# Optimization experiments

Hardware: AMD Instinct MI355X
Metric: run time of the kernel (lower is better)

## Reference

```python
import jax, jax.numpy as jnp
import numpy as np

BATCH, T, IN_DIM = 256, 1024, 96
N_UNITS, N_CLASSES = 256, 10
EPS, BETA, GAMMA = 0.01, 0.5, 0.0


def setup_inputs() -> dict:
    key = jax.random.key(0)
    k = jax.random.split(key, 7)
    # Xavier-ish scales for linear layers; unit gaussian for C, B (gaussian_init_ std=1)
    return {
        "x":   jax.random.normal(k[0], (BATCH, T, IN_DIM), dtype=jnp.float32),
        "E_w": jax.random.normal(k[1], (N_UNITS, IN_DIM), dtype=jnp.float32) * (2.0 / (IN_DIM + N_UNITS)) ** 0.5,
        "E_b": jnp.zeros((N_UNITS,), dtype=jnp.float32),
        "C":   jax.random.normal(k[2], (N_UNITS, N_UNITS), dtype=jnp.float32) / N_UNITS ** 0.5,
        "B":   jax.random.normal(k[3], (N_UNITS, N_UNITS), dtype=jnp.float32) / N_UNITS ** 0.5,
        "D_w": jax.random.normal(k[4], (N_CLASSES, N_UNITS), dtype=jnp.float32) * (2.0 / (N_UNITS + N_CLASSES)) ** 0.5,
        "D_b": jnp.zeros((N_CLASSES,), dtype=jnp.float32),
    }


def reference(x, E_w, E_b, C, B, D_w, D_b):
    # Invariant recurrence matrices (the torch code rebuilds these every step)
    I = jnp.eye(N_UNITS, dtype=x.dtype)
    A  = BETA * (C - C.T) + (1.0 - BETA) * (C + C.T) - GAMMA * I
    Dm = BETA * (B - B.T) + (1.0 - BETA) * (B + B.T) - GAMMA * I

    # Input projection for all timesteps at once: [B, T, N]
    z = jnp.einsum("btf,nf->btn", x, E_w) + E_b

    def step(h, z_t):  # h: [B, N], z_t: [B, N]
        h = h + EPS * (h @ Dm) + EPS * jnp.tanh(h @ A + z_t)
        return h, None

    h0 = jnp.zeros((x.shape[0], N_UNITS), dtype=x.dtype)
    h, _ = jax.lax.scan(step, h0, jnp.swapaxes(z, 0, 1))  # scan over T

    return h @ D_w.T + D_b  # [B, n_classes]
```

## Files before the change

### kernel.cpp

```cpp
#include <hip/hip_runtime.h>

#define BATCH 256
#define TT 1024
#define IN_DIM 96
#define NU 256
#define NC 10
#define EPS 0.01f
#define BETA 0.5f
#define GAMMA 0.0f
#define TWOLOG2E 2.8853900817779268f

typedef _Float16 f16x8 __attribute__((ext_vector_type(8)));
typedef _Float16 f16x4 __attribute__((ext_vector_type(4)));
typedef float f32x4 __attribute__((ext_vector_type(4)));

#define ZP_BYTES ((size_t)TT * 16 * 16 * 256 * 2)
#define WSW_OFF  ZP_BYTES
#define WSW_BYTES ((size_t)16384 * 16)
#define ESW_OFF  (WSW_OFF + WSW_BYTES)

__global__ void prep_w(const float* __restrict__ C, const float* __restrict__ B,
                       _Float16* __restrict__ Wsw) {
    int u = blockIdx.x * 256 + threadIdx.x;
    int l = u & 63;
    int i = (u >> 6) & 1;
    int c = (u >> 7) & 7;
    int mat = (u >> 10) & 1;
    int w = u >> 11;
    int n = w * 32 + i * 16 + (l & 15);
    int kb = c * 32 + (l >> 4) * 8;
    const float* M = mat ? C : B;
    float scale = mat ? (16.0f * TWOLOG2E) : EPS;
    f16x8 v;
#pragma unroll
    for (int j = 0; j < 8; j++) {
        int k = kb + j;
        float m1 = M[k * NU + n];
        float m2 = M[n * NU + k];
        float val = BETA * (m1 - m2) + (1.0f - BETA) * (m1 + m2)
                    - ((k == n) ? GAMMA : 0.0f);
        v[j] = (_Float16)(val * scale);
    }
    ((f16x8*)Wsw)[u] = v;
}

__global__ void prep_e(const float* __restrict__ Ew, _Float16* __restrict__ Esw) {
    int u = blockIdx.x * 256 + threadIdx.x;
    int l = u & 63;
    int i = (u >> 6) & 3;
    int wc = u >> 8;
    int c = wc % 3;
    int w = wc / 3;
    int n = w * 64 + i * 16 + (l & 15);
    int kb = c * 32 + (l >> 4) * 8;
    f16x8 v;
#pragma unroll
    for (int j = 0; j < 8; j++)
        v[j] = (_Float16)(Ew[n * IN_DIM + kb + j] * TWOLOG2E);
    ((f16x8*)Esw)[u] = v;
}

__global__ __launch_bounds__(256) void zproj(const float* __restrict__ x,
                                             const float* __restrict__ Eb,
                                             const _Float16* __restrict__ Esw,
                                             _Float16* __restrict__ zp) {
    __shared__ __align__(16) _Float16 zt[2][16 * 264];
    int tid = threadIdx.x;
    int l = tid & 63, wz = tid >> 6, m = l & 15, q = l >> 4;
    int bb = blockIdx.x & 15, tb = blockIdx.x >> 4;
    int t0 = tb * 16, B0 = bb * 16;

    f16x8 ef[3][4];
    const f16x8* Ep = (const f16x8*)Esw;
#pragma unroll
    for (int c = 0; c < 3; c++)
#pragma unroll
        for (int i = 0; i < 4; i++)
            ef[c][i] = Ep[((wz * 3 + c) * 4 + i) * 64 + l];
    f32x4 ebv[4];
#pragma unroll
    for (int i = 0; i < 4; i++) {
        float4 b4 = *(const float4*)&Eb[wz * 64 + i * 16 + q * 4];
        f32x4 e4 = {b4.x * TWOLOG2E, b4.y * TWOLOG2E,
                    b4.z * TWOLOG2E, b4.w * TWOLOG2E};
        ebv[i] = e4;
    }

    const float* xbase = x + (size_t)(B0 + m) * TT * IN_DIM + q * 8;

    for (int t = 0; t < 16; t++) {
        f16x8 af[3];
#pragma unroll
        for (int c = 0; c < 3; c++) {
            const float* px = xbase + (size_t)(t0 + t) * IN_DIM + c * 32;
            float4 v0 = *(const float4*)px;
            float4 v1 = *(const float4*)(px + 4);
            f16x8 a;
            a[0] = (_Float16)v0.x; a[1] = (_Float16)v0.y;
            a[2] = (_Float16)v0.z; a[3] = (_Float16)v0.w;
            a[4] = (_Float16)v1.x; a[5] = (_Float16)v1.y;
            a[6] = (_Float16)v1.z; a[7] = (_Float16)v1.w;
            af[c] = a;
        }
        f32x4 acc[4];
#pragma unroll
        for (int i = 0; i < 4; i++) acc[i] = ebv[i];
#pragma unroll
        for (int c = 0; c < 3; c++)
#pragma unroll
            for (int i = 0; i < 4; i++)
                acc[i] = __builtin_amdgcn_mfma_f32_16x16x32_f16(ef[c][i], af[c], acc[i], 0, 0, 0);

        _Float16* zb = zt[t & 1];
#pragma unroll
        for (int i = 0; i < 4; i++) {
            f16x4 o = {(_Float16)acc[i][0], (_Float16)acc[i][1],
                       (_Float16)acc[i][2], (_Float16)acc[i][3]};
            *(f16x4*)&zb[m * 264 + wz * 64 + i * 16 + q * 4] = o;
        }
        __syncthreads();
        {
            const _Float16* src = &zb[(tid >> 4) * 264 + (tid & 15) * 16];
            f16x8 s0 = *(const f16x8*)src;
            f16x8 s1 = *(const f16x8*)(src + 8);
            _Float16* dst = zp + (((size_t)(t0 + t) * 16 + bb) * 4096) + tid * 16;
            *(f16x8*)dst = s0;
            *(f16x8*)(dst + 8) = s1;
        }
    }
}


__device__ __forceinline__ void load_z2(f16x4 zc[2][2],
                                        const _Float16* __restrict__ zp,
                                        int tb, int wg, size_t voff0, size_t voff1) {
#pragma unroll
    for (int s = 0; s < 2; s++) {
        int ts = tb + s; ts = (ts > TT - 1) ? TT - 1 : ts;
        const _Float16* pz = zp + ((size_t)ts * 16 + wg) * 4096;
        zc[s][0] = *(const f16x4*)(pz + voff0);
        zc[s][1] = *(const f16x4*)(pz + voff1);
    }
}

__device__ __forceinline__ void step_fn(const _Float16* __restrict__ hb,
                                        _Float16* __restrict__ hn,
                                        const f16x8 wd[8][2], const f16x8 wa[8][2],
                                        float hm[8], const f16x4 zs[2],
                                        int m, int q, int w) {
    f32x4 faccD[2], faccA[2];
    f32x4 dinit = {EPS * 0.0625f, EPS * 0.0625f, EPS * 0.0625f, EPS * 0.0625f};
#pragma unroll
    for (int i = 0; i < 2; i++) {
        faccD[i] = dinit;
        f32x4 zi = {(float)zs[i][0], (float)zs[i][1],
                    (float)zs[i][2], (float)zs[i][3]};
        faccA[i] = zi;
    }

#pragma unroll
    for (int c = 0; c < 8; c++) {
        f16x8 af = *(const f16x8*)&hb[m * 264 + c * 32 + q * 8];
#pragma unroll
        for (int i = 0; i < 2; i++) {
            faccD[i] = __builtin_amdgcn_mfma_f32_16x16x32_f16(wd[c][i], af, faccD[i], 0, 0, 0);
            faccA[i] = __builtin_amdgcn_mfma_f32_16x16x32_f16(wa[c][i], af, faccA[i], 0, 0, 0);
        }
    }

#pragma unroll
    for (int i = 0; i < 2; i++) {
        f16x4 o;
#pragma unroll
        for (int r = 0; r < 4; r++) {
            float e = __builtin_amdgcn_exp2f(faccA[i][r]);
            float R = __builtin_amdgcn_rcpf(e + 1.0f);
            float s = hm[i * 4 + r] + faccD[i][r];
            hm[i * 4 + r] = s - (2.0f * EPS * 0.0625f) * R;
            o[r] = (_Float16)hm[i * 4 + r];
        }
        *(f16x4*)&hn[m * 264 + w * 32 + i * 16 + q * 4] = o;
    }
    __syncthreads();
}

__global__ __launch_bounds__(512, 2) void recur(const _Float16* __restrict__ Wsw,
                                                const _Float16* __restrict__ zp,
                                                const float* __restrict__ Dw,
                                                const float* __restrict__ Db,
                                                float* __restrict__ out) {
    __shared__ __align__(16) _Float16 hbuf0[16 * 264];
    __shared__ __align__(16) _Float16 hbuf1[16 * 264];
    __shared__ float Yep[16 * 257];
    int tid = threadIdx.x;
    int l = tid & 63, w = tid >> 6, m = l & 15, q = l >> 4;
    int wg = blockIdx.x;

    f16x8 wd[8][2], wa[8][2];
    const f16x8* Wp = (const f16x8*)Wsw;
#pragma unroll
    for (int c = 0; c < 8; c++)
#pragma unroll
        for (int i = 0; i < 2; i++) {
            wd[c][i] = Wp[(((w * 2 + 0) * 8 + c) * 2 + i) * 64 + l];
            wa[c][i] = Wp[(((w * 2 + 1) * 8 + c) * 2 + i) * 64 + l];
        }
#pragma unroll
    for (int c = 0; c < 8; c++)
#pragma unroll
        for (int i = 0; i < 2; i++)
            asm volatile("" : "+v"(wd[c][i]), "+v"(wa[c][i]));

    float hm[8];
#pragma unroll
    for (int e = 0; e < 8; e++) hm[e] = 0.0f;
    for (int idx = tid; idx < 16 * 264; idx += 512) hbuf0[idx] = (_Float16)0.0f;

    size_t voff0 = (size_t)m * 256 + w * 32 + q * 4;
    size_t voff1 = voff0 + 16;
    f16x4 zA[2][2], zB[2][2];
    load_z2(zA, zp, 0, wg, voff0, voff1);
    load_z2(zB, zp, 2, wg, voff0, voff1);
    __syncthreads();

    for (int t = 0; t < TT; t += 4) {
        step_fn(hbuf0, hbuf1, wd, wa, hm, zA[0], m, q, w);
        step_fn(hbuf1, hbuf0, wd, wa, hm, zA[1], m, q, w);
        load_z2(zA, zp, t + 4, wg, voff0, voff1);
        step_fn(hbuf0, hbuf1, wd, wa, hm, zB[0], m, q, w);
        step_fn(hbuf1, hbuf0, wd, wa, hm, zB[1], m, q, w);
        load_z2(zB, zp, t + 6, wg, voff0, voff1);
    }

#pragma unroll
    for (int i = 0; i < 2; i++)
#pragma unroll
        for (int r = 0; r < 4; r++)
            Yep[m * 257 + w * 32 + i * 16 + q * 4 + r] = 16.0f * hm[i * 4 + r];
    __syncthreads();
    if (tid < 160) {
        int rr = tid / 10, c = tid - rr * 10;
        float s = Db[c];
        for (int k = 0; k < 256; k++) s += Yep[rr * 257 + k] * Dw[c * 256 + k];
        out[(wg * 16 + rr) * 10 + c] = s;
    }
}

extern "C" void kernel_launch(void* const* d_in, const int* in_sizes, int n_in,
                              void* d_out, int out_size, void* d_ws, size_t ws_size,
                              hipStream_t stream) {
    const float* x  = (const float*)d_in[0];
    const float* Ew = (const float*)d_in[1];
    const float* Eb = (const float*)d_in[2];
    const float* C  = (const float*)d_in[3];
    const float* B  = (const float*)d_in[4];
    const float* Dw = (const float*)d_in[5];
    const float* Db = (const float*)d_in[6];
    float* out = (float*)d_out;

    char* ws = (char*)d_ws;
    _Float16* zp  = (_Float16*)(ws);
    _Float16* Wsw = (_Float16*)(ws + WSW_OFF);
    _Float16* Esw = (_Float16*)(ws + ESW_OFF);

    hipLaunchKernelGGL(prep_w, dim3(64), dim3(256), 0, stream, C, B, Wsw);
    hipLaunchKernelGGL(prep_e, dim3(12), dim3(256), 0, stream, Ew, Esw);
    hipLaunchKernelGGL(zproj, dim3(1024), dim3(256), 0, stream, x, Eb, Esw, zp);
    hipLaunchKernelGGL(recur, dim3(16), dim3(512), 0, stream, Wsw, zp, Dw, Db, out);
}
```

Before: 1.131 ms.

## Use 4 waves per recurrence block with permuted K layout and vectorized stores

The recurrence kernel drops from 8 to 4 waves per block, so each wave owns 64 output columns and keeps twice as many weight fragments in registers. The K dimension of the weights is permuted so each lane's MFMA outputs land contiguously, which lets h and z be stored and loaded as 16-byte vectors. zproj writes results straight to global memory in the matching permuted layout instead of staging them through shared memory. The step barrier becomes a raw s_barrier with an explicit lgkmcnt wait. Fewer waves means fewer barrier participants per step, at the cost of less latency hiding and higher register pressure.

```diff
diff --git a/kernel.cpp b/kernel.cpp
--- a/kernel.cpp
+++ b/kernel.cpp
@@ -19,22 +19,25 @@
 #define WSW_BYTES ((size_t)16384 * 16)
 #define ESW_OFF  (WSW_OFF + WSW_BYTES)
 
+
 __global__ void prep_w(const float* __restrict__ C, const float* __restrict__ B,
                        _Float16* __restrict__ Wsw) {
     int u = blockIdx.x * 256 + threadIdx.x;
     int l = u & 63;
-    int i = (u >> 6) & 1;
-    int c = (u >> 7) & 7;
-    int mat = (u >> 10) & 1;
-    int w = u >> 11;
-    int n = w * 32 + i * 16 + (l & 15);
+    int i = (u >> 6) & 3;
+    int c = (u >> 8) & 7;
+    int mat = (u >> 11) & 1;
+    int w = u >> 12;
+    int n = w * 64 + i * 16 + (l & 15);
     int kb = c * 32 + (l >> 4) * 8;
     const float* M = mat ? C : B;
     float scale = mat ? (16.0f * TWOLOG2E) : EPS;
     f16x8 v;
 #pragma unroll
     for (int j = 0; j < 8; j++) {
-        int k = kb + j;
+        int kk = kb + j;
+        int k = (kk >> 6) * 64 + ((kk >> 2) & 3) * 16
+              + ((kk >> 4) & 3) * 4 + (kk & 3);
         float m1 = M[k * NU + n];
         float m2 = M[n * NU + k];
         float val = BETA * (m1 - m2) + (1.0f - BETA) * (m1 + m2)
@@ -64,7 +67,6 @@
                                              const float* __restrict__ Eb,
                                              const _Float16* __restrict__ Esw,
                                              _Float16* __restrict__ zp) {
-    __shared__ __align__(16) _Float16 zt[2][16 * 264];
     int tid = threadIdx.x;
     int l = tid & 63, wz = tid >> 6, m = l & 15, q = l >> 4;
     int bb = blockIdx.x & 15, tb = blockIdx.x >> 4;
@@ -111,50 +113,48 @@
             for (int i = 0; i < 4; i++)
                 acc[i] = __builtin_amdgcn_mfma_f32_16x16x32_f16(ef[c][i], af[c], acc[i], 0, 0, 0);
 
-        _Float16* zb = zt[t & 1];
-#pragma unroll
-        for (int i = 0; i < 4; i++) {
-            f16x4 o = {(_Float16)acc[i][0], (_Float16)acc[i][1],
-                       (_Float16)acc[i][2], (_Float16)acc[i][3]};
-            *(f16x4*)&zb[m * 264 + wz * 64 + i * 16 + q * 4] = o;
-        }
-        __syncthreads();
-        {
-            const _Float16* src = &zb[(tid >> 4) * 264 + (tid & 15) * 16];
-            f16x8 s0 = *(const f16x8*)src;
-            f16x8 s1 = *(const f16x8*)(src + 8);
-            _Float16* dst = zp + (((size_t)(t0 + t) * 16 + bb) * 4096) + tid * 16;
-            *(f16x8*)dst = s0;
-            *(f16x8*)(dst + 8) = s1;
-        }
-    }
-}
-
-
-__device__ __forceinline__ void load_z2(f16x4 zc[2][2],
+        f16x8 o0, o1;
+#pragma unroll
+        for (int r = 0; r < 4; r++) {
+            o0[r]     = (_Float16)acc[0][r];
+            o0[4 + r] = (_Float16)acc[1][r];
+            o1[r]     = (_Float16)acc[2][r];
+            o1[4 + r] = (_Float16)acc[3][r];
+        }
+        _Float16* dst = zp + (((size_t)(t0 + t) * 16 + bb) * 4096)
+                        + ((size_t)((wz * 16 + m) * 4 + q)) * 16;
+        *(f16x8*)dst = o0;
+        *(f16x8*)(dst + 8) = o1;
+    }
+}
+
+
+__device__ __forceinline__ void load_z2(f16x8 zc[2][2],
                                         const _Float16* __restrict__ zp,
-                                        int tb, int wg, size_t voff0, size_t voff1) {
+                                        int tb, int wg, size_t voff) {
 #pragma unroll
     for (int s = 0; s < 2; s++) {
         int ts = tb + s; ts = (ts > TT - 1) ? TT - 1 : ts;
-        const _Float16* pz = zp + ((size_t)ts * 16 + wg) * 4096;
-        zc[s][0] = *(const f16x4*)(pz + voff0);
-        zc[s][1] = *(const f16x4*)(pz + voff1);
+        const _Float16* pz = zp + ((size_t)ts * 16 + wg) * 4096 + voff;
+        zc[s][0] = *(const f16x8*)pz;
+        zc[s][1] = *(const f16x8*)(pz + 8);
     }
 }
 
 __device__ __forceinline__ void step_fn(const _Float16* __restrict__ hb,
                                         _Float16* __restrict__ hn,
-                                        const f16x8 wd[8][2], const f16x8 wa[8][2],
-                                        float hm[8], const f16x4 zs[2],
+                                        const f16x8 wd[8][4], const f16x8 wa[8][4],
+                                        float hm[16], const f16x8 zs[2],
                                         int m, int q, int w) {
-    f32x4 faccD[2], faccA[2];
+    f32x4 faccD[4], faccA[4];
     f32x4 dinit = {EPS * 0.0625f, EPS * 0.0625f, EPS * 0.0625f, EPS * 0.0625f};
 #pragma unroll
-    for (int i = 0; i < 2; i++) {
+    for (int i = 0; i < 4; i++) {
         faccD[i] = dinit;
-        f32x4 zi = {(float)zs[i][0], (float)zs[i][1],
-                    (float)zs[i][2], (float)zs[i][3]};
+        f32x4 zi = {(float)zs[i >> 1][(i & 1) * 4 + 0],
+                    (float)zs[i >> 1][(i & 1) * 4 + 1],
+                    (float)zs[i >> 1][(i & 1) * 4 + 2],
+                    (float)zs[i >> 1][(i & 1) * 4 + 3]};
         faccA[i] = zi;
     }
 
@@ -162,29 +162,36 @@
     for (int c = 0; c < 8; c++) {
         f16x8 af = *(const f16x8*)&hb[m * 264 + c * 32 + q * 8];
 #pragma unroll
-        for (int i = 0; i < 2; i++) {
+        for (int i = 0; i < 4; i++) {
             faccD[i] = __builtin_amdgcn_mfma_f32_16x16x32_f16(wd[c][i], af, faccD[i], 0, 0, 0);
             faccA[i] = __builtin_amdgcn_mfma_f32_16x16x32_f16(wa[c][i], af, faccA[i], 0, 0, 0);
         }
     }
 
-#pragma unroll
-    for (int i = 0; i < 2; i++) {
-        f16x4 o;
+    f16x8 o0, o1;
+#pragma unroll
+    for (int i = 0; i < 4; i++) {
 #pragma unroll
         for (int r = 0; r < 4; r++) {
             float e = __builtin_amdgcn_exp2f(faccA[i][r]);
             float R = __builtin_amdgcn_rcpf(e + 1.0f);
             float s = hm[i * 4 + r] + faccD[i][r];
             hm[i * 4 + r] = s - (2.0f * EPS * 0.0625f) * R;
-            o[r] = (_Float16)hm[i * 4 + r];
-        }
-        *(f16x4*)&hn[m * 264 + w * 32 + i * 16 + q * 4] = o;
-    }
-    __syncthreads();
-}
-
-__global__ __launch_bounds__(512, 2) void recur(const _Float16* __restrict__ Wsw,
+            _Float16 hv = (_Float16)hm[i * 4 + r];
+            if (i < 2) o0[(i & 1) * 4 + r] = hv;
+            else       o1[(i & 1) * 4 + r] = hv;
+        }
+    }
+    _Float16* dst = &hn[m * 264 + w * 64 + q * 16];
+    *(f16x8*)dst = o0;
+    *(f16x8*)(dst + 8) = o1;
+
+    asm volatile("s_waitcnt lgkmcnt(0)" ::: "memory");
+    __builtin_amdgcn_s_barrier();
+    __builtin_amdgcn_sched_barrier(0);
+}
+
+__global__ __launch_bounds__(256, 1) void recur(const _Float16* __restrict__ Wsw,
                                                 const _Float16* __restrict__ zp,
                                                 const float* __restrict__ Dw,
                                                 const float* __restrict__ Db,
@@ -196,47 +203,46 @@
     int l = tid & 63, w = tid >> 6, m = l & 15, q = l >> 4;
     int wg = blockIdx.x;
 
-    f16x8 wd[8][2], wa[8][2];
+    f16x8 wd[8][4], wa[8][4];
     const f16x8* Wp = (const f16x8*)Wsw;
 #pragma unroll
     for (int c = 0; c < 8; c++)
 #pragma unroll
-        for (int i = 0; i < 2; i++) {
-            wd[c][i] = Wp[(((w * 2 + 0) * 8 + c) * 2 + i) * 64 + l];
-            wa[c][i] = Wp[(((w * 2 + 1) * 8 + c) * 2 + i) * 64 + l];
+        for (int i = 0; i < 4; i++) {
+            wd[c][i] = Wp[(((w * 2 + 0) * 8 + c) * 4 + i) * 64 + l];
+            wa[c][i] = Wp[(((w * 2 + 1) * 8 + c) * 4 + i) * 64 + l];
         }
 #pragma unroll
     for (int c = 0; c < 8; c++)
 #pragma unroll
-        for (int i = 0; i < 2; i++)
+        for (int i = 0; i < 4; i++)
             asm volatile("" : "+v"(wd[c][i]), "+v"(wa[c][i]));
 
-    float hm[8];
-#pragma unroll
-    for (int e = 0; e < 8; e++) hm[e] = 0.0f;
-    for (int idx = tid; idx < 16 * 264; idx += 512) hbuf0[idx] = (_Float16)0.0f;
-
-    size_t voff0 = (size_t)m * 256 + w * 32 + q * 4;
-    size_t voff1 = voff0 + 16;
-    f16x4 zA[2][2], zB[2][2];
-    load_z2(zA, zp, 0, wg, voff0, voff1);
-    load_z2(zB, zp, 2, wg, voff0, voff1);
+    float hm[16];
+#pragma unroll
+    for (int e = 0; e < 16; e++) hm[e] = 0.0f;
+    for (int idx = tid; idx < 16 * 264; idx += 256) hbuf0[idx] = (_Float16)0.0f;
+
+    size_t voff = (size_t)((w * 16 + m) * 4 + q) * 16;
+    f16x8 zA[2][2], zB[2][2];
+    load_z2(zA, zp, 0, wg, voff);
+    load_z2(zB, zp, 2, wg, voff);
     __syncthreads();
 
     for (int t = 0; t < TT; t += 4) {
         step_fn(hbuf0, hbuf1, wd, wa, hm, zA[0], m, q, w);
         step_fn(hbuf1, hbuf0, wd, wa, hm, zA[1], m, q, w);
-        load_z2(zA, zp, t + 4, wg, voff0, voff1);
+        load_z2(zA, zp, t + 4, wg, voff);
         step_fn(hbuf0, hbuf1, wd, wa, hm, zB[0], m, q, w);
         step_fn(hbuf1, hbuf0, wd, wa, hm, zB[1], m, q, w);
-        load_z2(zB, zp, t + 6, wg, voff0, voff1);
-    }
-
-#pragma unroll
-    for (int i = 0; i < 2; i++)
+        load_z2(zB, zp, t + 6, wg, voff);
+    }
+
+#pragma unroll
+    for (int i = 0; i < 4; i++)
 #pragma unroll
         for (int r = 0; r < 4; r++)
-            Yep[m * 257 + w * 32 + i * 16 + q * 4 + r] = 16.0f * hm[i * 4 + r];
+            Yep[m * 257 + w * 64 + i * 16 + q * 4 + r] = 16.0f * hm[i * 4 + r];
     __syncthreads();
     if (tid < 160) {
         int rr = tid / 10, c = tid - rr * 10;
@@ -266,5 +272,5 @@
     hipLaunchKernelGGL(prep_w, dim3(64), dim3(256), 0, stream, C, B, Wsw);
     hipLaunchKernelGGL(prep_e, dim3(12), dim3(256), 0, stream, Ew, Esw);
     hipLaunchKernelGGL(zproj, dim3(1024), dim3(256), 0, stream, x, Eb, Esw, zp);
-    hipLaunchKernelGGL(recur, dim3(16), dim3(512), 0, stream, Wsw, zp, Dw, Db, out);
-}
+    hipLaunchKernelGGL(recur, dim3(16), dim3(256), 0, stream, Wsw, zp, Dw, Db, out);
+}
```

Result: slower. 1.170 ms (+3.4%).

## Interleave two batch tiles per recurrence block and permute K for vector I/O

Applied to the files above, without the earlier changes.

Each recurrence workgroup now advances two independent 16-row batch tiles at once, interleaving their MFMA chains so each tile's latency hides behind the other's, and uses one barrier per pair of steps. This halves the grid to 8 blocks. The K dimension of the weights is permuted so each lane's hidden-state outputs are contiguous, allowing single 16-byte LDS stores and 16-byte z loads. zproj writes directly to global in the new layout, dropping its LDS staging and barrier. The cost is fewer active CUs and more register pressure.

```diff
diff --git a/kernel.cpp b/kernel.cpp
--- a/kernel.cpp
+++ b/kernel.cpp
@@ -18,6 +18,7 @@
 #define WSW_OFF  ZP_BYTES
 #define WSW_BYTES ((size_t)16384 * 16)
 #define ESW_OFF  (WSW_OFF + WSW_BYTES)
+
 
 __global__ void prep_w(const float* __restrict__ C, const float* __restrict__ B,
                        _Float16* __restrict__ Wsw) {
@@ -34,7 +35,9 @@
     f16x8 v;
 #pragma unroll
     for (int j = 0; j < 8; j++) {
-        int k = kb + j;
+        int kk = kb + j;
+        int k = (kk >> 5) * 32 + ((kk >> 2) & 1) * 16
+              + ((kk >> 3) & 3) * 4 + (kk & 3);
         float m1 = M[k * NU + n];
         float m2 = M[n * NU + k];
         float val = BETA * (m1 - m2) + (1.0f - BETA) * (m1 + m2)
@@ -64,7 +67,6 @@
                                              const float* __restrict__ Eb,
                                              const _Float16* __restrict__ Esw,
                                              _Float16* __restrict__ zp) {
-    __shared__ __align__(16) _Float16 zt[2][16 * 264];
     int tid = threadIdx.x;
     int l = tid & 63, wz = tid >> 6, m = l & 15, q = l >> 4;
     int bb = blockIdx.x & 15, tb = blockIdx.x >> 4;
@@ -111,77 +113,80 @@
             for (int i = 0; i < 4; i++)
                 acc[i] = __builtin_amdgcn_mfma_f32_16x16x32_f16(ef[c][i], af[c], acc[i], 0, 0, 0);
 
-        _Float16* zb = zt[t & 1];
-#pragma unroll
-        for (int i = 0; i < 4; i++) {
-            f16x4 o = {(_Float16)acc[i][0], (_Float16)acc[i][1],
-                       (_Float16)acc[i][2], (_Float16)acc[i][3]};
-            *(f16x4*)&zb[m * 264 + wz * 64 + i * 16 + q * 4] = o;
-        }
-        __syncthreads();
-        {
-            const _Float16* src = &zb[(tid >> 4) * 264 + (tid & 15) * 16];
-            f16x8 s0 = *(const f16x8*)src;
-            f16x8 s1 = *(const f16x8*)(src + 8);
-            _Float16* dst = zp + (((size_t)(t0 + t) * 16 + bb) * 4096) + tid * 16;
-            *(f16x8*)dst = s0;
-            *(f16x8*)(dst + 8) = s1;
-        }
-    }
-}
-
-
-__device__ __forceinline__ void load_z2(f16x4 zc[2][2],
-                                        const _Float16* __restrict__ zp,
-                                        int tb, int wg, size_t voff0, size_t voff1) {
-#pragma unroll
-    for (int s = 0; s < 2; s++) {
-        int ts = tb + s; ts = (ts > TT - 1) ? TT - 1 : ts;
-        const _Float16* pz = zp + ((size_t)ts * 16 + wg) * 4096;
-        zc[s][0] = *(const f16x4*)(pz + voff0);
-        zc[s][1] = *(const f16x4*)(pz + voff1);
-    }
-}
-
-__device__ __forceinline__ void step_fn(const _Float16* __restrict__ hb,
-                                        _Float16* __restrict__ hn,
-                                        const f16x8 wd[8][2], const f16x8 wa[8][2],
-                                        float hm[8], const f16x4 zs[2],
-                                        int m, int q, int w) {
-    f32x4 faccD[2], faccA[2];
-    f32x4 dinit = {EPS * 0.0625f, EPS * 0.0625f, EPS * 0.0625f, EPS * 0.0625f};
+        f16x8 o0, o1;
+#pragma unroll
+        for (int r = 0; r < 4; r++) {
+            o0[r]     = (_Float16)acc[0][r];
+            o0[4 + r] = (_Float16)acc[1][r];
+            o1[r]     = (_Float16)acc[2][r];
+            o1[4 + r] = (_Float16)acc[3][r];
+        }
+        _Float16* slab = zp + (((size_t)(t0 + t) * 16 + bb) * 4096);
+        *(f16x8*)(slab + ((size_t)(((2 * wz) * 16 + m) * 4 + q)) * 8)     = o0;
+        *(f16x8*)(slab + ((size_t)(((2 * wz + 1) * 16 + m) * 4 + q)) * 8) = o1;
+    }
+}
+
+
+__device__ __forceinline__ f16x8 load_z1(const _Float16* __restrict__ zp,
+                                         int ts, int bb, size_t voff) {
+    ts = (ts > TT - 1) ? TT - 1 : ts;
+    return *(const f16x8*)(zp + ((size_t)ts * 16 + bb) * 4096 + voff);
+}
+
+__device__ __forceinline__ void epi_store(const f32x4 faccD[2], const f32x4 faccA[2],
+                                          float hm[8], _Float16* __restrict__ hn,
+                                          int m, int q, int w) {
+    f16x8 o;
 #pragma unroll
     for (int i = 0; i < 2; i++) {
-        faccD[i] = dinit;
-        f32x4 zi = {(float)zs[i][0], (float)zs[i][1],
-                    (float)zs[i][2], (float)zs[i][3]};
-        faccA[i] = zi;
-    }
-
-#pragma unroll
-    for (int c = 0; c < 8; c++) {
-        f16x8 af = *(const f16x8*)&hb[m * 264 + c * 32 + q * 8];
-#pragma unroll
-        for (int i = 0; i < 2; i++) {
-            faccD[i] = __builtin_amdgcn_mfma_f32_16x16x32_f16(wd[c][i], af, faccD[i], 0, 0, 0);
-            faccA[i] = __builtin_amdgcn_mfma_f32_16x16x32_f16(wa[c][i], af, faccA[i], 0, 0, 0);
-        }
-    }
-
-#pragma unroll
-    for (int i = 0; i < 2; i++) {
-        f16x4 o;
 #pragma unroll
         for (int r = 0; r < 4; r++) {
             float e = __builtin_amdgcn_exp2f(faccA[i][r]);
             float R = __builtin_amdgcn_rcpf(e + 1.0f);
             float s = hm[i * 4 + r] + faccD[i][r];
             hm[i * 4 + r] = s - (2.0f * EPS * 0.0625f) * R;
-            o[r] = (_Float16)hm[i * 4 + r];
-        }
-        *(f16x4*)&hn[m * 264 + w * 32 + i * 16 + q * 4] = o;
-    }
-    __syncthreads();
+            o[i * 4 + r] = (_Float16)hm[i * 4 + r];
+        }
+    }
+    *(f16x8*)&hn[m * 264 + w * 32 + q * 8] = o;
+}
+
+__device__ __forceinline__ void stepAB(const _Float16* __restrict__ hbA,
+                                       _Float16* __restrict__ hnA,
+                                       const _Float16* __restrict__ hbB,
+                                       _Float16* __restrict__ hnB,
+                                       const f16x8 wd[8][2], const f16x8 wa[8][2],
+                                       float hmA[8], float hmB[8],
+                                       f16x8 zA, f16x8 zB,
+                                       int m, int q, int w) {
+    f32x4 fDA[2], fAA[2], fDB[2], fAB[2];
+    f32x4 dinit = {EPS * 0.0625f, EPS * 0.0625f, EPS * 0.0625f, EPS * 0.0625f};
+#pragma unroll
+    for (int i = 0; i < 2; i++) {
+        fDA[i] = dinit;  fDB[i] = dinit;
+        f32x4 za = {(float)zA[i * 4 + 0], (float)zA[i * 4 + 1],
+                    (float)zA[i * 4 + 2], (float)zA[i * 4 + 3]};
+        f32x4 zb = {(float)zB[i * 4 + 0], (float)zB[i * 4 + 1],
+                    (float)zB[i * 4 + 2], (float)zB[i * 4 + 3]};
+        fAA[i] = za;  fAB[i] = zb;
+    }
+
+#pragma unroll
+    for (int c = 0; c < 8; c++) {
+        f16x8 afA = *(const f16x8*)&hbA[m * 264 + c * 32 + q * 8];
+        f16x8 afB = *(const f16x8*)&hbB[m * 264 + c * 32 + q * 8];
+#pragma unroll
+        for (int i = 0; i < 2; i++) {
+            fDA[i] = __builtin_amdgcn_mfma_f32_16x16x32_f16(wd[c][i], afA, fDA[i], 0, 0, 0);
+            fAA[i] = __builtin_amdgcn_mfma_f32_16x16x32_f16(wa[c][i], afA, fAA[i], 0, 0, 0);
+            fDB[i] = __builtin_amdgcn_mfma_f32_16x16x32_f16(wd[c][i], afB, fDB[i], 0, 0, 0);
+            fAB[i] = __builtin_amdgcn_mfma_f32_16x16x32_f16(wa[c][i], afB, fAB[i], 0, 0, 0);
+        }
+    }
+
+    epi_store(fDA, fAA, hmA, hnA, m, q, w);
+    epi_store(fDB, fAB, hmB, hnB, m, q, w);
 }
 
 __global__ __launch_bounds__(512, 2) void recur(const _Float16* __restrict__ Wsw,
@@ -189,12 +194,15 @@
                                                 const float* __restrict__ Dw,
                                                 const float* __restrict__ Db,
                                                 float* __restrict__ out) {
-    __shared__ __align__(16) _Float16 hbuf0[16 * 264];
-    __shared__ __align__(16) _Float16 hbuf1[16 * 264];
+    __shared__ __align__(16) _Float16 hA0[16 * 264];
+    __shared__ __align__(16) _Float16 hA1[16 * 264];
+    __shared__ __align__(16) _Float16 hB0[16 * 264];
+    __shared__ __align__(16) _Float16 hB1[16 * 264];
     __shared__ float Yep[16 * 257];
     int tid = threadIdx.x;
     int l = tid & 63, w = tid >> 6, m = l & 15, q = l >> 4;
     int wg = blockIdx.x;
+    int bbA = wg * 2, bbB = wg * 2 + 1;
 
     f16x8 wd[8][2], wa[8][2];
     const f16x8* Wp = (const f16x8*)Wsw;
@@ -211,38 +219,62 @@
         for (int i = 0; i < 2; i++)
             asm volatile("" : "+v"(wd[c][i]), "+v"(wa[c][i]));
 
-    float hm[8];
-#pragma unroll
-    for (int e = 0; e < 8; e++) hm[e] = 0.0f;
-    for (int idx = tid; idx < 16 * 264; idx += 512) hbuf0[idx] = (_Float16)0.0f;
-
-    size_t voff0 = (size_t)m * 256 + w * 32 + q * 4;
-    size_t voff1 = voff0 + 16;
-    f16x4 zA[2][2], zB[2][2];
-    load_z2(zA, zp, 0, wg, voff0, voff1);
-    load_z2(zB, zp, 2, wg, voff0, voff1);
-    __syncthreads();
-
-    for (int t = 0; t < TT; t += 4) {
-        step_fn(hbuf0, hbuf1, wd, wa, hm, zA[0], m, q, w);
-        step_fn(hbuf1, hbuf0, wd, wa, hm, zA[1], m, q, w);
-        load_z2(zA, zp, t + 4, wg, voff0, voff1);
-        step_fn(hbuf0, hbuf1, wd, wa, hm, zB[0], m, q, w);
-        step_fn(hbuf1, hbuf0, wd, wa, hm, zB[1], m, q, w);
-        load_z2(zB, zp, t + 6, wg, voff0, voff1);
-    }
-
+    float hmA[8], hmB[8];
+#pragma unroll
+    for (int e = 0; e < 8; e++) { hmA[e] = 0.0f; hmB[e] = 0.0f; }
+    for (int idx = tid; idx < 16 * 264; idx += 512) {
+        hA0[idx] = (_Float16)0.0f;
+        hB0[idx] = (_Float16)0.0f;
+    }
+
+    size_t voff = (size_t)((w * 16 + m) * 4 + q) * 8;
+    f16x8 zA0 = load_z1(zp, 0, bbA, voff);
+    f16x8 zB0 = load_z1(zp, 0, bbB, voff);
+    f16x8 zA1 = load_z1(zp, 1, bbA, voff);
+    f16x8 zB1 = load_z1(zp, 1, bbB, voff);
+    __syncthreads();
+
+    for (int t = 0; t < TT; t += 2) {
+        stepAB(hA0, hA1, hB0, hB1, wd, wa, hmA, hmB, zA0, zB0, m, q, w);
+        zA0 = load_z1(zp, t + 2, bbA, voff);
+        zB0 = load_z1(zp, t + 2, bbB, voff);
+        asm volatile("s_waitcnt lgkmcnt(0)" ::: "memory");
+        __builtin_amdgcn_s_barrier();
+        __builtin_amdgcn_sched_barrier(0);
+
+        stepAB(hA1, hA0, hB1, hB0, wd, wa, hmA, hmB, zA1, zB1, m, q, w);
+        zA1 = load_z1(zp, t + 3, bbA, voff);
+        zB1 = load_z1(zp, t + 3, bbB, voff);
+        asm volatile("s_waitcnt lgkmcnt(0)" ::: "memory");
+        __builtin_amdgcn_s_barrier();
+        __builtin_amdgcn_sched_barrier(0);
+    }
+
+    __syncthreads();
 #pragma unroll
     for (int i = 0; i < 2; i++)
 #pragma unroll
         for (int r = 0; r < 4; r++)
-            Yep[m * 257 + w * 32 + i * 16 + q * 4 + r] = 16.0f * hm[i * 4 + r];
+            Yep[m * 257 + w * 32 + i * 16 + q * 4 + r] = 16.0f * hmA[i * 4 + r];
     __syncthreads();
     if (tid < 160) {
         int rr = tid / 10, c = tid - rr * 10;
         float s = Db[c];
         for (int k = 0; k < 256; k++) s += Yep[rr * 257 + k] * Dw[c * 256 + k];
-        out[(wg * 16 + rr) * 10 + c] = s;
+        out[(bbA * 16 + rr) * 10 + c] = s;
+    }
+    __syncthreads();
+#pragma unroll
+    for (int i = 0; i < 2; i++)
+#pragma unroll
+        for (int r = 0; r < 4; r++)
+            Yep[m * 257 + w * 32 + i * 16 + q * 4 + r] = 16.0f * hmB[i * 4 + r];
+    __syncthreads();
+    if (tid < 160) {
+        int rr = tid / 10, c = tid - rr * 10;
+        float s = Db[c];
+        for (int k = 0; k < 256; k++) s += Yep[rr * 257 + k] * Dw[c * 256 + k];
+        out[(bbB * 16 + rr) * 10 + c] = s;
     }
 }
 
@@ -266,5 +298,5 @@
     hipLaunchKernelGGL(prep_w, dim3(64), dim3(256), 0, stream, C, B, Wsw);
     hipLaunchKernelGGL(prep_e, dim3(12), dim3(256), 0, stream, Ew, Esw);
     hipLaunchKernelGGL(zproj, dim3(1024), dim3(256), 0, stream, x, Eb, Esw, zp);
-    hipLaunchKernelGGL(recur, dim3(16), dim3(512), 0, stream, Wsw, zp, Dw, Db, out);
-}
+    hipLaunchKernelGGL(recur, dim3(8), dim3(512), 0, stream, Wsw, zp, Dw, Db, out);
+}
```

New measurement: 1.559 ms. 37.8% more time.

## Permute K-dim in weights so hidden state and z use 16-byte vector accesses

Applied to the files above, without the earlier changes.

Permutes the K index of the recurrence weight matrices so each lane's two 16-row output tiles become contiguous 8-halfword chunks. Each lane can then write h with a single 16-byte LDS store and read z with a single 16-byte global load. The zproj kernel writes z straight to global in the new per-lane layout, dropping its LDS staging buffer and barrier. The per-step __syncthreads is replaced by an explicit lgkmcnt wait, s_barrier and sched_barrier, so the z prefetch can stay in flight across the barrier, with a deeper 4-step prefetch.

```diff
diff --git a/kernel.cpp b/kernel.cpp
--- a/kernel.cpp
+++ b/kernel.cpp
@@ -18,6 +18,7 @@
 #define WSW_OFF  ZP_BYTES
 #define WSW_BYTES ((size_t)16384 * 16)
 #define ESW_OFF  (WSW_OFF + WSW_BYTES)
+
 
 __global__ void prep_w(const float* __restrict__ C, const float* __restrict__ B,
                        _Float16* __restrict__ Wsw) {
@@ -34,7 +35,9 @@
     f16x8 v;
 #pragma unroll
     for (int j = 0; j < 8; j++) {
-        int k = kb + j;
+        int kk = kb + j;
+        int k = (kk >> 5) * 32 + ((kk >> 2) & 1) * 16
+              + ((kk >> 3) & 3) * 4 + (kk & 3);
         float m1 = M[k * NU + n];
         float m2 = M[n * NU + k];
         float val = BETA * (m1 - m2) + (1.0f - BETA) * (m1 + m2)
@@ -64,7 +67,6 @@
                                              const float* __restrict__ Eb,
                                              const _Float16* __restrict__ Esw,
                                              _Float16* __restrict__ zp) {
-    __shared__ __align__(16) _Float16 zt[2][16 * 264];
     int tid = threadIdx.x;
     int l = tid & 63, wz = tid >> 6, m = l & 15, q = l >> 4;
     int bb = blockIdx.x & 15, tb = blockIdx.x >> 4;
@@ -111,50 +113,39 @@
             for (int i = 0; i < 4; i++)
                 acc[i] = __builtin_amdgcn_mfma_f32_16x16x32_f16(ef[c][i], af[c], acc[i], 0, 0, 0);
 
-        _Float16* zb = zt[t & 1];
-#pragma unroll
-        for (int i = 0; i < 4; i++) {
-            f16x4 o = {(_Float16)acc[i][0], (_Float16)acc[i][1],
-                       (_Float16)acc[i][2], (_Float16)acc[i][3]};
-            *(f16x4*)&zb[m * 264 + wz * 64 + i * 16 + q * 4] = o;
-        }
-        __syncthreads();
-        {
-            const _Float16* src = &zb[(tid >> 4) * 264 + (tid & 15) * 16];
-            f16x8 s0 = *(const f16x8*)src;
-            f16x8 s1 = *(const f16x8*)(src + 8);
-            _Float16* dst = zp + (((size_t)(t0 + t) * 16 + bb) * 4096) + tid * 16;
-            *(f16x8*)dst = s0;
-            *(f16x8*)(dst + 8) = s1;
-        }
-    }
-}
-
-
-__device__ __forceinline__ void load_z2(f16x4 zc[2][2],
-                                        const _Float16* __restrict__ zp,
-                                        int tb, int wg, size_t voff0, size_t voff1) {
-#pragma unroll
-    for (int s = 0; s < 2; s++) {
-        int ts = tb + s; ts = (ts > TT - 1) ? TT - 1 : ts;
-        const _Float16* pz = zp + ((size_t)ts * 16 + wg) * 4096;
-        zc[s][0] = *(const f16x4*)(pz + voff0);
-        zc[s][1] = *(const f16x4*)(pz + voff1);
-    }
+        f16x8 o0, o1;
+#pragma unroll
+        for (int r = 0; r < 4; r++) {
+            o0[r]     = (_Float16)acc[0][r];
+            o0[4 + r] = (_Float16)acc[1][r];
+            o1[r]     = (_Float16)acc[2][r];
+            o1[4 + r] = (_Float16)acc[3][r];
+        }
+        _Float16* slab = zp + (((size_t)(t0 + t) * 16 + bb) * 4096);
+        *(f16x8*)(slab + ((size_t)(((2 * wz) * 16 + m) * 4 + q)) * 8)     = o0;
+        *(f16x8*)(slab + ((size_t)(((2 * wz + 1) * 16 + m) * 4 + q)) * 8) = o1;
+    }
+}
+
+
+__device__ __forceinline__ f16x8 load_z1(const _Float16* __restrict__ zp,
+                                         int ts, int bb, size_t voff) {
+    ts = (ts > TT - 1) ? TT - 1 : ts;
+    return *(const f16x8*)(zp + ((size_t)ts * 16 + bb) * 4096 + voff);
 }
 
 __device__ __forceinline__ void step_fn(const _Float16* __restrict__ hb,
                                         _Float16* __restrict__ hn,
                                         const f16x8 wd[8][2], const f16x8 wa[8][2],
-                                        float hm[8], const f16x4 zs[2],
+                                        float hm[8], f16x8 zs,
                                         int m, int q, int w) {
     f32x4 faccD[2], faccA[2];
     f32x4 dinit = {EPS * 0.0625f, EPS * 0.0625f, EPS * 0.0625f, EPS * 0.0625f};
 #pragma unroll
     for (int i = 0; i < 2; i++) {
         faccD[i] = dinit;
-        f32x4 zi = {(float)zs[i][0], (float)zs[i][1],
-                    (float)zs[i][2], (float)zs[i][3]};
+        f32x4 zi = {(float)zs[i * 4 + 0], (float)zs[i * 4 + 1],
+                    (float)zs[i * 4 + 2], (float)zs[i * 4 + 3]};
         faccA[i] = zi;
     }
 
@@ -168,21 +159,25 @@
         }
     }
 
+    f16x8 o;
 #pragma unroll
     for (int i = 0; i < 2; i++) {
-        f16x4 o;
 #pragma unroll
         for (int r = 0; r < 4; r++) {
             float e = __builtin_amdgcn_exp2f(faccA[i][r]);
             float R = __builtin_amdgcn_rcpf(e + 1.0f);
             float s = hm[i * 4 + r] + faccD[i][r];
             hm[i * 4 + r] = s - (2.0f * EPS * 0.0625f) * R;
-            o[r] = (_Float16)hm[i * 4 + r];
-        }
-        *(f16x4*)&hn[m * 264 + w * 32 + i * 16 + q * 4] = o;
-    }
-    __syncthreads();
-}
+            o[i * 4 + r] = (_Float16)hm[i * 4 + r];
+        }
+    }
+    *(f16x8*)&hn[m * 264 + w * 32 + q * 8] = o;
+}
+
+#define STEP_SYNC()                                          \
+    asm volatile("s_waitcnt lgkmcnt(0)" ::: "memory");       \
+    __builtin_amdgcn_s_barrier();                            \
+    __builtin_amdgcn_sched_barrier(0)
 
 __global__ __launch_bounds__(512, 2) void recur(const _Float16* __restrict__ Wsw,
                                                 const _Float16* __restrict__ zp,
@@ -216,20 +211,26 @@
     for (int e = 0; e < 8; e++) hm[e] = 0.0f;
     for (int idx = tid; idx < 16 * 264; idx += 512) hbuf0[idx] = (_Float16)0.0f;
 
-    size_t voff0 = (size_t)m * 256 + w * 32 + q * 4;
-    size_t voff1 = voff0 + 16;
-    f16x4 zA[2][2], zB[2][2];
-    load_z2(zA, zp, 0, wg, voff0, voff1);
-    load_z2(zB, zp, 2, wg, voff0, voff1);
+    size_t voff = (size_t)((w * 16 + m) * 4 + q) * 8;
+    f16x8 z0 = load_z1(zp, 0, wg, voff);
+    f16x8 z1 = load_z1(zp, 1, wg, voff);
+    f16x8 z2 = load_z1(zp, 2, wg, voff);
+    f16x8 z3 = load_z1(zp, 3, wg, voff);
     __syncthreads();
 
     for (int t = 0; t < TT; t += 4) {
-        step_fn(hbuf0, hbuf1, wd, wa, hm, zA[0], m, q, w);
-        step_fn(hbuf1, hbuf0, wd, wa, hm, zA[1], m, q, w);
-        load_z2(zA, zp, t + 4, wg, voff0, voff1);
-        step_fn(hbuf0, hbuf1, wd, wa, hm, zB[0], m, q, w);
-        step_fn(hbuf1, hbuf0, wd, wa, hm, zB[1], m, q, w);
-        load_z2(zB, zp, t + 6, wg, voff0, voff1);
+        step_fn(hbuf0, hbuf1, wd, wa, hm, z0, m, q, w);
+        z0 = load_z1(zp, t + 4, wg, voff);
+        STEP_SYNC();
+        step_fn(hbuf1, hbuf0, wd, wa, hm, z1, m, q, w);
+        z1 = load_z1(zp, t + 5, wg, voff);
+        STEP_SYNC();
+        step_fn(hbuf0, hbuf1, wd, wa, hm, z2, m, q, w);
+        z2 = load_z1(zp, t + 6, wg, voff);
+        STEP_SYNC();
+        step_fn(hbuf1, hbuf0, wd, wa, hm, z3, m, q, w);
+        z3 = load_z1(zp, t + 7, wg, voff);
+        STEP_SYNC();
     }
 
 #pragma unroll
```

Result: faster. 934.5 us (-17.4%).
